# Optimization experiments

Hardware: AMD Instinct MI355X
Metric: run time of the kernel (lower is better)

Reference implementation:

```python
import jax, jax.numpy as jnp
import numpy as np

# MoE config (matches init_kwargs): dim=512, num_experts=16, top_k=2, ffn mult=4
DIM = 512
NUM_EXPERTS = 16
TOP_K = 2
HIDDEN = 4 * DIM  # FeedForward inner dim
TOKENS = 2048
LN_EPS = 1e-5


def setup_inputs() -> dict:
    key = jax.random.key(0)
    ks = jax.random.split(key, 4)
    scaled = lambda k, shape, fan_in: (
        jax.random.normal(k, shape, dtype=jnp.float32) / np.sqrt(fan_in)
    )
    return {
        "x": jax.random.normal(ks[0], (TOKENS, DIM), dtype=jnp.float32),
        # gate: Linear(dim, num_experts, bias=False)
        "Wg": scaled(ks[1], (DIM, NUM_EXPERTS), DIM),
        # per-expert FFN params stacked on leading expert axis
        "W1": scaled(ks[2], (NUM_EXPERTS, DIM, HIDDEN), DIM),
        "b1": jnp.zeros((NUM_EXPERTS, HIDDEN), jnp.float32),
        "ln_g": jnp.ones((NUM_EXPERTS, HIDDEN), jnp.float32),
        "ln_b": jnp.zeros((NUM_EXPERTS, HIDDEN), jnp.float32),
        "W2": scaled(ks[3], (NUM_EXPERTS, HIDDEN, DIM), HIDDEN),
        "b2": jnp.zeros((NUM_EXPERTS, DIM), jnp.float32),
    }


def reference(x, Wg, W1, b1, ln_g, ln_b, W2, b2):
    # ---- routing ----
    gate_logits = x @ Wg                                   # [T, E]
    w, sel = jax.lax.top_k(gate_logits, TOP_K)             # [T, k]
    # softmax over the selected-experts axis, computed in fp32 (matches dtype=torch.float)
    w = jax.nn.softmax(w.astype(jnp.float32), axis=-1).astype(x.dtype)
    n_exp = Wg.shape[1]
    # combine[t, e] = sum_k w[t, k] * 1[sel[t, k] == e]
    combine = jnp.sum(
        w[..., None] * jax.nn.one_hot(sel, n_exp, dtype=x.dtype), axis=1
    )                                                      # [T, E]

    # ---- all experts (dense, jit-friendly dispatch) ----
    # FeedForward: Linear -> SiLU -> LayerNorm -> (Dropout=identity at eval) -> Linear
    h = jnp.einsum("td,edh->eth", x, W1) + b1[:, None, :]  # [E, T, H]
    h = jax.nn.silu(h)
    mu = jnp.mean(h, axis=-1, keepdims=True)
    var = jnp.mean(jnp.square(h - mu), axis=-1, keepdims=True)
    h = (h - mu) * jax.lax.rsqrt(var + LN_EPS)
    h = h * ln_g[:, None, :] + ln_b[:, None, :]
    y = jnp.einsum("eth,ehd->etd", h, W2) + b2[:, None, :]  # [E, T, D]

    # ---- weighted combine (scatter-add equivalent) ----
    return jnp.einsum("etd,te->td", y, combine)             # [T, D]
```

## Files before the change

kernel.cpp:

```cpp
#include <hip/hip_runtime.h>
#include <hip/hip_bf16.h>

#define TOKENS 2048
#define DIM 512
#define NEXP 16
#define HID 2048
#define CAP 320
#define NTPE (CAP / 64)
#define MTILES (NEXP * NTPE)
#define NROWS (NEXP * CAP)

typedef unsigned short ushort_t;
typedef __attribute__((ext_vector_type(8))) __bf16 bf16x8;
typedef __attribute__((ext_vector_type(4))) float f32x4;

#define OFF_CNT 0
#define OFF_LTOK 1024
#define OFF_LW 21504
#define OFF_S1 41984
#define OFF_S2 62464
#define OFF_XBF 82944
#define OFF_H 2180096
#define OFF_W1T 23151616
#define OFF_W2T 56706048

__device__ __forceinline__ ushort_t f2b(float f) {
  __bf16 b = (__bf16)f;
  return __builtin_bit_cast(unsigned short, b);
}
__device__ __forceinline__ float b2f(ushort_t u) {
  return __builtin_bit_cast(float, (unsigned)u << 16);
}


__global__ __launch_bounds__(256) void pre_k(
    const float* __restrict__ x, const float* __restrict__ Wg,
    const float* __restrict__ W1, ushort_t* __restrict__ xbf,
    int* __restrict__ counts, int* __restrict__ ltok, float* __restrict__ lw,
    float* __restrict__ s1, float* __restrict__ s2, float* __restrict__ out,
    ushort_t* __restrict__ W1t) {
  int bid = blockIdx.x;
  int t = threadIdx.x;
  if (bid >= 64) {
    int idx = bid - 64;
    int xcd = idx & 7;
    int j = idx >> 3;
    int e = ((j >> 8) << 3) | xcd;
    int bx = j & 255;
    int bn = bx & 31, bk = bx >> 5;
    const int K = DIM, N = HID;
    int w = t >> 6, l = t & 63;
    int n = bn * 64 + l;
    int k_base = bk * 64, kt0 = k_base >> 5, kk = w * 8;
    const float* sp = W1 + ((size_t)e * K + k_base + kk) * N + n;
    float v[16];
#pragma unroll
    for (int jj = 0; jj < 8; jj++)
      v[jj] = __builtin_nontemporal_load(sp + (size_t)jj * N);
#pragma unroll
    for (int jj = 0; jj < 8; jj++)
      v[8 + jj] = __builtin_nontemporal_load(sp + (size_t)(32 + jj) * N);
    size_t tb = ((size_t)(e * (N >> 4) + (n >> 4)) * (K >> 5) + kt0) * 512 +
                (n & 15) * 32 + kk;
    union { ushort_t u[8]; uint4 q; } s0, s1u;
#pragma unroll
    for (int jj = 0; jj < 8; jj++) { s0.u[jj] = f2b(v[jj]); s1u.u[jj] = f2b(v[8 + jj]); }
    *(uint4*)(W1t + tb) = s0.q;
    *(uint4*)(W1t + tb + 512) = s1u.q;
    return;
  }

  {
    float4 z = {0.f, 0.f, 0.f, 0.f};
    float4* o4 = (float4*)out + bid * 4096 + t;
#pragma unroll
    for (int i = 0; i < 16; i++) o4[i * 256] = z;
  }
  {
    int idx = bid * 256 + t;
    if (idx < NROWS) { s1[idx] = 0.f; s2[idx] = 0.f; }
  }

  __shared__ float xs[4][512];
  __shared__ float lg[4][16];
  __shared__ int lcnt[NEXP];
  __shared__ int ltoks[NEXP][64];
  __shared__ float lws[NEXP][64];
  __shared__ int base_s[NEXP];

  if (t < NEXP) lcnt[t] = 0;
  __syncthreads();

  int lane = t & 63, w = t >> 6;
  int dq = lane >> 2, e4 = lane & 3;
  const float* wgp = Wg + dq * NEXP + e4 * 4;

  for (int it = 0; it < 8; it++) {
    int tok = bid * 32 + w * 8 + it;
    const float* xr = x + (size_t)tok * DIM + lane * 8;
    float4 xa = *(const float4*)xr;
    float4 xb = *(const float4*)(xr + 4);
    union { ushort_t u[8]; uint4 v; } pk;
    pk.u[0] = f2b(xa.x); pk.u[1] = f2b(xa.y); pk.u[2] = f2b(xa.z); pk.u[3] = f2b(xa.w);
    pk.u[4] = f2b(xb.x); pk.u[5] = f2b(xb.y); pk.u[6] = f2b(xb.z); pk.u[7] = f2b(xb.w);
    *(uint4*)(xbf + (size_t)tok * DIM + lane * 8) = pk.v;
    *(float4*)&xs[w][lane * 8] = xa;
    *(float4*)&xs[w][lane * 8 + 4] = xb;

    float4 a = {0.f, 0.f, 0.f, 0.f};
#pragma unroll
    for (int kk = 0; kk < 32; kk++) {
      float xv = xs[w][kk * 16 + dq];
      float4 g = *(const float4*)(wgp + kk * 16 * NEXP);
      a.x += xv * g.x; a.y += xv * g.y; a.z += xv * g.z; a.w += xv * g.w;
    }
#pragma unroll
    for (int off = 32; off >= 4; off >>= 1) {
      a.x += __shfl_down(a.x, off);
      a.y += __shfl_down(a.y, off);
      a.z += __shfl_down(a.z, off);
      a.w += __shfl_down(a.w, off);
    }
    if (lane < 4) *(float4*)&lg[w][lane * 4] = a;
    if (lane == 0) {
      int i0 = 0;
      float v0 = lg[w][0];
#pragma unroll
      for (int e = 1; e < NEXP; e++)
        if (lg[w][e] > v0) { v0 = lg[w][e]; i0 = e; }
      int i1 = -1;
      float v1 = -3.4e38f;
#pragma unroll
      for (int e = 0; e < NEXP; e++)
        if (e != i0 && lg[w][e] > v1) { v1 = lg[w][e]; i1 = e; }
      float ex = __expf(v1 - v0);
      float w0 = 1.f / (1.f + ex);
      int p0 = atomicAdd(&lcnt[i0], 1);
      ltoks[i0][p0] = tok;
      lws[i0][p0] = w0;
      int p1 = atomicAdd(&lcnt[i1], 1);
      ltoks[i1][p1] = tok;
      lws[i1][p1] = ex / (1.f + ex);
    }
  }
  __syncthreads();
  if (t < NEXP) base_s[t] = atomicAdd(&counts[t], lcnt[t]);
  __syncthreads();
  int e = t >> 4, i0 = t & 15;
  int n = lcnt[e], b = base_s[e];
  for (int i = i0; i < n; i += 16) {
    int slot = b + i;
    if (slot < CAP) {
      ltok[e * CAP + slot] = ltoks[e][i];
      lw[e * CAP + slot] = lws[e][i];
    }
  }
}

__global__ __launch_bounds__(256) void mid_k(
    const ushort_t* __restrict__ W1t, const float* __restrict__ b1,
    const int* __restrict__ counts, const int* __restrict__ ltok,
    const ushort_t* __restrict__ xbf, ushort_t* __restrict__ hbuf,
    float* __restrict__ s1, float* __restrict__ s2,
    const float* __restrict__ W2, ushort_t* __restrict__ W2t) {
  int bid = blockIdx.x;
  int t = threadIdx.x;
  if (bid >= 640) {
    int idx = bid - 640;
    int xcd = idx & 7;
    int j = idx >> 3;
    int e = ((j >> 8) << 3) | xcd;
    int bx = j & 255;
    int bn = bx & 7, bk = bx >> 3;
    const int K = HID, N = DIM;
    int w = t >> 6, l = t & 63;
    int n = bn * 64 + l;
    int k_base = bk * 64, kt0 = k_base >> 5, kk = w * 8;
    const float* sp = W2 + ((size_t)e * K + k_base + kk) * N + n;
    float v[16];
#pragma unroll
    for (int jj = 0; jj < 8; jj++)
      v[jj] = __builtin_nontemporal_load(sp + (size_t)jj * N);
#pragma unroll
    for (int jj = 0; jj < 8; jj++)
      v[8 + jj] = __builtin_nontemporal_load(sp + (size_t)(32 + jj) * N);
    size_t tb = ((size_t)(e * (N >> 4) + (n >> 4)) * (K >> 5) + kt0) * 512 +
                (n & 15) * 32 + kk;
    union { ushort_t u[8]; uint4 q; } s0, s1u;
#pragma unroll
    for (int jj = 0; jj < 8; jj++) { s0.u[jj] = f2b(v[jj]); s1u.u[jj] = f2b(v[8 + jj]); }
    *(uint4*)(W2t + tb) = s0.q;
    *(uint4*)(W2t + tb + 512) = s1u.q;
    return;
  }

  int xcd = bid & 7;
  int j = bid >> 3;
  int e = ((j / 40) << 3) | xcd;
  int r = j % 40;
  int mt = r >> 3;
  int h0 = (r & 7) * 256;
  int cnt = counts[e];
  if (cnt - mt * 64 <= 0) return;
  int row0 = e * CAP + mt * 64;

  __shared__ __align__(16) ushort_t As[2][64 * 40];

  int lane = t & 63, wave = t >> 6;
  int quad = lane >> 4, l16 = lane & 15;

  int sr = t >> 2, sp = t & 3;
  int stok = ltok[row0 + sr];
  bool sok = (unsigned)stok < TOKENS;
  const ushort_t* sx = xbf + (size_t)(sok ? stok : 0) * DIM + sp * 8;

  int ncol = h0 + wave * 64 + l16;
  const ushort_t* bb = W1t +
      ((size_t)(e * 128 + (h0 >> 4) + wave * 4) * 16) * 512 + l16 * 32 + quad * 8;

  f32x4 acc[4][4];
#pragma unroll
  for (int a = 0; a < 4; a++)
#pragma unroll
    for (int b = 0; b < 4; b++) acc[a][b] = {0.f, 0.f, 0.f, 0.f};

  uint4 avB = {0u, 0u, 0u, 0u};
  {
    uint4 avA = {0u, 0u, 0u, 0u};
    if (sok) {
      avA = *(const uint4*)(sx);
      avB = *(const uint4*)(sx + 32);
    }
    *(uint4*)(&As[0][sr * 40 + sp * 8]) = avA;
  }
  bf16x8 bc[4];
#pragma unroll
  for (int nb = 0; nb < 4; nb++)
    bc[nb] = *(const bf16x8*)(bb + nb * 8192);

#pragma unroll
  for (int ks = 0; ks < 16; ks++) {
    __syncthreads();
    bf16x8 bn[4];
    if (ks < 15) {
#pragma unroll
      for (int nb = 0; nb < 4; nb++)
        bn[nb] = *(const bf16x8*)(bb + nb * 8192 + (ks + 1) * 512);
    }
    uint4 avN = {0u, 0u, 0u, 0u};
    if (ks < 14 && sok) avN = *(const uint4*)(sx + (ks + 2) * 32);

    bf16x8 af[4];
#pragma unroll
    for (int mb = 0; mb < 4; mb++)
      af[mb] = *(const bf16x8*)(&As[ks & 1][(mb * 16 + l16) * 40 + quad * 8]);
#pragma unroll
    for (int mb = 0; mb < 4; mb++)
#pragma unroll
      for (int nb = 0; nb < 4; nb++)
        acc[mb][nb] = __builtin_amdgcn_mfma_f32_16x16x32_bf16(af[mb], bc[nb], acc[mb][nb], 0, 0, 0);

    if (ks < 15) {
      *(uint4*)(&As[(ks + 1) & 1][sr * 40 + sp * 8]) = avB;
      avB = avN;
#pragma unroll
      for (int nb = 0; nb < 4; nb++) bc[nb] = bn[nb];
    }
  }

  float bia[4];
#pragma unroll
  for (int nb = 0; nb < 4; nb++) bia[nb] = b1[e * HID + ncol + nb * 16];
#pragma unroll
  for (int mb = 0; mb < 4; mb++) {
#pragma unroll
    for (int i = 0; i < 4; i++) {
      int m = mb * 16 + quad * 4 + i;
      size_t rowg = (size_t)(row0 + m);
      float ps = 0.f, qs = 0.f;
#pragma unroll
      for (int nb = 0; nb < 4; nb++) {
        float v = acc[mb][nb][i] + bia[nb];
        v = v / (1.f + __expf(-v));
        hbuf[rowg * HID + ncol + nb * 16] = f2b(v);
        ps += v;
        qs += v * v;
      }
      ps += __shfl_down(ps, 8); qs += __shfl_down(qs, 8);
      ps += __shfl_down(ps, 4); qs += __shfl_down(qs, 4);
      ps += __shfl_down(ps, 2); qs += __shfl_down(qs, 2);
      ps += __shfl_down(ps, 1); qs += __shfl_down(qs, 1);
      if (l16 == 0) {
        atomicAdd(&s1[rowg], ps);
        atomicAdd(&s2[rowg], qs);
      }
    }
  }
}

__global__ __launch_bounds__(256) void ffn2_k(
    const ushort_t* __restrict__ W2t, const float* __restrict__ b2,
    const float* __restrict__ lng, const float* __restrict__ lnb,
    const int* __restrict__ counts, const int* __restrict__ ltok,
    const float* __restrict__ lw, const ushort_t* __restrict__ hbuf,
    const float* __restrict__ s1, const float* __restrict__ s2,
    float* __restrict__ out) {
  int bid = blockIdx.x;
  int xcd = bid & 7, j = bid >> 3;
  int eh = j / 40, r = j % 40;
  int e = (eh << 3) | xcd;
  int mt = r % 5, yz = r / 5;
  int n0 = (yz >> 1) * 128;
  int z = yz & 1;
  int kbeg = z * (HID / 2);

  int cnt = counts[e];
  int valid = cnt - mt * 64;
  if (valid <= 0) return;
  valid = valid > 64 ? 64 : valid;
  int row0 = e * CAP + mt * 64;

  __shared__ __align__(16) ushort_t As[2][64 * 40];
  __shared__ float Gs[1024];
  __shared__ float Cs[1024];

  int t = threadIdx.x;
  int lane = t & 63, wave = t >> 6;
  int quad = lane >> 4, l16 = lane & 15;

  *(float4*)&Gs[t * 4] = *(const float4*)(lng + (size_t)e * HID + kbeg + t * 4);
  *(float4*)&Cs[t * 4] = *(const float4*)(lnb + (size_t)e * HID + kbeg + t * 4);

  int sr = t >> 2, sp = t & 3;
  size_t srow = (size_t)(row0 + sr);
  const ushort_t* hr = hbuf + srow * HID + kbeg + sp * 8;
  float smu = s1[srow] * (1.f / HID);
  float var = s2[srow] * (1.f / HID) - smu * smu;
  float srs = rsqrtf(var + 1e-5f);

  int ncol = n0 + wave * 32 + l16;
  const ushort_t* bb = W2t +
      ((size_t)(e * 32 + (n0 >> 4) + wave * 2) * 64 + z * 32) * 512 +
      l16 * 32 + quad * 8;

  f32x4 acc[4][2];
#pragma unroll
  for (int a = 0; a < 4; a++)
#pragma unroll
    for (int b = 0; b < 2; b++) acc[a][b] = {0.f, 0.f, 0.f, 0.f};

  uint4 hvA = *(const uint4*)(hr);
  uint4 hvB = *(const uint4*)(hr + 32);
  __syncthreads();

  {
    union { uint4 v; ushort_t u[8]; } hv;
    hv.v = hvA;
    int sb = sp * 8;
    union { ushort_t u[8]; uint4 v; } pk;
#pragma unroll
    for (int jj = 0; jj < 8; jj++) {
      float f = (b2f(hv.u[jj]) - smu) * srs;
      pk.u[jj] = f2b(f * Gs[sb + jj] + Cs[sb + jj]);
    }
    *(uint4*)(&As[0][sr * 40 + sp * 8]) = pk.v;
  }
  bf16x8 bc[2];
#pragma unroll
  for (int nb = 0; nb < 2; nb++)
    bc[nb] = *(const bf16x8*)(bb + nb * 32768);

#pragma unroll 8
  for (int ks = 0; ks < 32; ks++) {
    __syncthreads();
    bf16x8 bn[2];
    if (ks < 31) {
#pragma unroll
      for (int nb = 0; nb < 2; nb++)
        bn[nb] = *(const bf16x8*)(bb + nb * 32768 + (ks + 1) * 512);
    }
    uint4 hvN = {0u, 0u, 0u, 0u};
    if (ks < 30) hvN = *(const uint4*)(hr + (ks + 2) * 32);

    bf16x8 af[4];
#pragma unroll
    for (int mb = 0; mb < 4; mb++)
      af[mb] = *(const bf16x8*)(&As[ks & 1][(mb * 16 + l16) * 40 + quad * 8]);
#pragma unroll
    for (int mb = 0; mb < 4; mb++)
#pragma unroll
      for (int nb = 0; nb < 2; nb++)
        acc[mb][nb] = __builtin_amdgcn_mfma_f32_16x16x32_bf16(af[mb], bc[nb], acc[mb][nb], 0, 0, 0);

    if (ks < 31) {
      union { uint4 v; ushort_t u[8]; } hv;
      hv.v = hvB;
      int sb = (ks + 1) * 32 + sp * 8;
      union { ushort_t u[8]; uint4 v; } pk;
#pragma unroll
      for (int jj = 0; jj < 8; jj++) {
        float f = (b2f(hv.u[jj]) - smu) * srs;
        pk.u[jj] = f2b(f * Gs[sb + jj] + Cs[sb + jj]);
      }
      *(uint4*)(&As[(ks + 1) & 1][sr * 40 + sp * 8]) = pk.v;
      hvB = hvN;
#pragma unroll
      for (int nb = 0; nb < 2; nb++) bc[nb] = bn[nb];
    }
  }

  bool addb = (z == 0);
  float bia[2];
#pragma unroll
  for (int nb = 0; nb < 2; nb++)
    bia[nb] = addb ? b2[e * DIM + ncol + nb * 16] : 0.f;
#pragma unroll
  for (int mb = 0; mb < 4; mb++) {
#pragma unroll
    for (int i = 0; i < 4; i++) {
      int m = mb * 16 + quad * 4 + i;
      if (m < valid) {
        int tok = ltok[row0 + m];
        float w = lw[row0 + m];
#pragma unroll
        for (int nb = 0; nb < 2; nb++) {
          float v = acc[mb][nb][i] + bia[nb];
          atomicAdd(out + (size_t)tok * DIM + ncol + nb * 16, w * v);
        }
      }
    }
  }
}

extern "C" void kernel_launch(void* const* d_in, const int* in_sizes, int n_in,
                              void* d_out, int out_size, void* d_ws, size_t ws_size,
                              hipStream_t stream) {
  const float* x = (const float*)d_in[0];
  const float* Wg = (const float*)d_in[1];
  const float* W1 = (const float*)d_in[2];
  const float* b1 = (const float*)d_in[3];
  const float* lng = (const float*)d_in[4];
  const float* lnb = (const float*)d_in[5];
  const float* W2 = (const float*)d_in[6];
  const float* b2 = (const float*)d_in[7];
  float* out = (float*)d_out;

  char* ws = (char*)d_ws;
  int* counts = (int*)(ws + OFF_CNT);
  int* ltok = (int*)(ws + OFF_LTOK);
  float* lw = (float*)(ws + OFF_LW);
  float* s1 = (float*)(ws + OFF_S1);
  float* s2 = (float*)(ws + OFF_S2);
  ushort_t* xbf = (ushort_t*)(ws + OFF_XBF);
  ushort_t* hbuf = (ushort_t*)(ws + OFF_H);
  ushort_t* W1t = (ushort_t*)(ws + OFF_W1T);
  ushort_t* W2t = (ushort_t*)(ws + OFF_W2T);

  hipMemsetAsync(counts, 0, NEXP * sizeof(int), stream);
  pre_k<<<64 + 4096, 256, 0, stream>>>(x, Wg, W1, xbf, counts, ltok, lw,
                                       s1, s2, out, W1t);
  mid_k<<<640 + 4096, 256, 0, stream>>>(W1t, b1, counts, ltok, xbf, hbuf,
                                        s1, s2, W2, W2t);
  ffn2_k<<<640, 256, 0, stream>>>(W2t, b2, lng, lnb, counts, ltok, lw,
                                  hbuf, s1, s2, out);
}
```

Before: 235.0 us.

## Read fp32 expert weights directly in GEMMs, drop separate bf16 repack passes

Removes the blocks that converted W1 and W2 from fp32 to a tiled bf16 layout in workspace. The FFN GEMM kernels now load fp32 weights straight from the input with strided per-column loads and convert to bf16 in registers before the MFMA. This cuts a full write plus re-read of both weight tensors (about 128MB fp32 read, 64MB bf16 written then read). The cost is uncoalesced-ish strided scalar loads, more VGPRs for the fp32 prefetch buffers, and each weight element being read by several M-tiles in fp32 rather than bf16.

```diff
diff --git a/kernel.cpp b/kernel.cpp
--- a/kernel.cpp
+++ b/kernel.cpp
@@ -7,7 +7,6 @@
 #define HID 2048
 #define CAP 320
 #define NTPE (CAP / 64)
-#define MTILES (NEXP * NTPE)
 #define NROWS (NEXP * CAP)
 
 typedef unsigned short ushort_t;
@@ -21,8 +20,6 @@
 #define OFF_S2 62464
 #define OFF_XBF 82944
 #define OFF_H 2180096
-#define OFF_W1T 23151616
-#define OFF_W2T 56706048
 
 __device__ __forceinline__ ushort_t f2b(float f) {
   __bf16 b = (__bf16)f;
@@ -33,51 +30,20 @@
 }
 
 
-__global__ __launch_bounds__(256) void pre_k(
+__global__ __launch_bounds__(256) void router_k(
     const float* __restrict__ x, const float* __restrict__ Wg,
-    const float* __restrict__ W1, ushort_t* __restrict__ xbf,
-    int* __restrict__ counts, int* __restrict__ ltok, float* __restrict__ lw,
-    float* __restrict__ s1, float* __restrict__ s2, float* __restrict__ out,
-    ushort_t* __restrict__ W1t) {
-  int bid = blockIdx.x;
+    ushort_t* __restrict__ xbf, int* __restrict__ counts,
+    int* __restrict__ ltok, float* __restrict__ lw,
+    float* __restrict__ s1, float* __restrict__ s2, float* __restrict__ out) {
   int t = threadIdx.x;
-  if (bid >= 64) {
-    int idx = bid - 64;
-    int xcd = idx & 7;
-    int j = idx >> 3;
-    int e = ((j >> 8) << 3) | xcd;
-    int bx = j & 255;
-    int bn = bx & 31, bk = bx >> 5;
-    const int K = DIM, N = HID;
-    int w = t >> 6, l = t & 63;
-    int n = bn * 64 + l;
-    int k_base = bk * 64, kt0 = k_base >> 5, kk = w * 8;
-    const float* sp = W1 + ((size_t)e * K + k_base + kk) * N + n;
-    float v[16];
-#pragma unroll
-    for (int jj = 0; jj < 8; jj++)
-      v[jj] = __builtin_nontemporal_load(sp + (size_t)jj * N);
-#pragma unroll
-    for (int jj = 0; jj < 8; jj++)
-      v[8 + jj] = __builtin_nontemporal_load(sp + (size_t)(32 + jj) * N);
-    size_t tb = ((size_t)(e * (N >> 4) + (n >> 4)) * (K >> 5) + kt0) * 512 +
-                (n & 15) * 32 + kk;
-    union { ushort_t u[8]; uint4 q; } s0, s1u;
-#pragma unroll
-    for (int jj = 0; jj < 8; jj++) { s0.u[jj] = f2b(v[jj]); s1u.u[jj] = f2b(v[8 + jj]); }
-    *(uint4*)(W1t + tb) = s0.q;
-    *(uint4*)(W1t + tb + 512) = s1u.q;
-    return;
-  }
-
   {
     float4 z = {0.f, 0.f, 0.f, 0.f};
-    float4* o4 = (float4*)out + bid * 4096 + t;
+    float4* o4 = (float4*)out + blockIdx.x * 4096 + t;
 #pragma unroll
     for (int i = 0; i < 16; i++) o4[i * 256] = z;
   }
   {
-    int idx = bid * 256 + t;
+    int idx = blockIdx.x * 256 + t;
     if (idx < NROWS) { s1[idx] = 0.f; s2[idx] = 0.f; }
   }
 
@@ -96,7 +62,7 @@
   const float* wgp = Wg + dq * NEXP + e4 * 4;
 
   for (int it = 0; it < 8; it++) {
-    int tok = bid * 32 + w * 8 + it;
+    int tok = blockIdx.x * 32 + w * 8 + it;
     const float* xr = x + (size_t)tok * DIM + lane * 8;
     float4 xa = *(const float4*)xr;
     float4 xb = *(const float4*)(xr + 4);
@@ -157,43 +123,13 @@
   }
 }
 
-__global__ __launch_bounds__(256) void mid_k(
-    const ushort_t* __restrict__ W1t, const float* __restrict__ b1,
+__global__ __launch_bounds__(256) void ffn1_k(
+    const float* __restrict__ W1, const float* __restrict__ b1,
     const int* __restrict__ counts, const int* __restrict__ ltok,
     const ushort_t* __restrict__ xbf, ushort_t* __restrict__ hbuf,
-    float* __restrict__ s1, float* __restrict__ s2,
-    const float* __restrict__ W2, ushort_t* __restrict__ W2t) {
+    float* __restrict__ s1, float* __restrict__ s2) {
   int bid = blockIdx.x;
   int t = threadIdx.x;
-  if (bid >= 640) {
-    int idx = bid - 640;
-    int xcd = idx & 7;
-    int j = idx >> 3;
-    int e = ((j >> 8) << 3) | xcd;
-    int bx = j & 255;
-    int bn = bx & 7, bk = bx >> 3;
-    const int K = HID, N = DIM;
-    int w = t >> 6, l = t & 63;
-    int n = bn * 64 + l;
-    int k_base = bk * 64, kt0 = k_base >> 5, kk = w * 8;
-    const float* sp = W2 + ((size_t)e * K + k_base + kk) * N + n;
-    float v[16];
-#pragma unroll
-    for (int jj = 0; jj < 8; jj++)
-      v[jj] = __builtin_nontemporal_load(sp + (size_t)jj * N);
-#pragma unroll
-    for (int jj = 0; jj < 8; jj++)
-      v[8 + jj] = __builtin_nontemporal_load(sp + (size_t)(32 + jj) * N);
-    size_t tb = ((size_t)(e * (N >> 4) + (n >> 4)) * (K >> 5) + kt0) * 512 +
-                (n & 15) * 32 + kk;
-    union { ushort_t u[8]; uint4 q; } s0, s1u;
-#pragma unroll
-    for (int jj = 0; jj < 8; jj++) { s0.u[jj] = f2b(v[jj]); s1u.u[jj] = f2b(v[8 + jj]); }
-    *(uint4*)(W2t + tb) = s0.q;
-    *(uint4*)(W2t + tb + 512) = s1u.q;
-    return;
-  }
-
   int xcd = bid & 7;
   int j = bid >> 3;
   int e = ((j / 40) << 3) | xcd;
@@ -215,8 +151,7 @@
   const ushort_t* sx = xbf + (size_t)(sok ? stok : 0) * DIM + sp * 8;
 
   int ncol = h0 + wave * 64 + l16;
-  const ushort_t* bb = W1t +
-      ((size_t)(e * 128 + (h0 >> 4) + wave * 4) * 16) * 512 + l16 * 32 + quad * 8;
+  const float* wb = W1 + ((size_t)e * DIM + quad * 8) * HID + ncol;
 
   f32x4 acc[4][4];
 #pragma unroll
@@ -233,22 +168,35 @@
     }
     *(uint4*)(&As[0][sr * 40 + sp * 8]) = avA;
   }
-  bf16x8 bc[4];
+  float bcf[4][8];
 #pragma unroll
   for (int nb = 0; nb < 4; nb++)
-    bc[nb] = *(const bf16x8*)(bb + nb * 8192);
+#pragma unroll
+    for (int jj = 0; jj < 8; jj++)
+      bcf[nb][jj] = wb[(size_t)jj * HID + nb * 16];
 
 #pragma unroll
   for (int ks = 0; ks < 16; ks++) {
     __syncthreads();
-    bf16x8 bn[4];
+    float bnf[4][8];
     if (ks < 15) {
 #pragma unroll
       for (int nb = 0; nb < 4; nb++)
-        bn[nb] = *(const bf16x8*)(bb + nb * 8192 + (ks + 1) * 512);
+#pragma unroll
+        for (int jj = 0; jj < 8; jj++)
+          bnf[nb][jj] = wb[(size_t)((ks + 1) * 32 + jj) * HID + nb * 16];
     }
     uint4 avN = {0u, 0u, 0u, 0u};
     if (ks < 14 && sok) avN = *(const uint4*)(sx + (ks + 2) * 32);
+
+    bf16x8 bc[4];
+#pragma unroll
+    for (int nb = 0; nb < 4; nb++) {
+      union { ushort_t u[8]; bf16x8 f; } o;
+#pragma unroll
+      for (int jj = 0; jj < 8; jj++) o.u[jj] = f2b(bcf[nb][jj]);
+      bc[nb] = o.f;
+    }
 
     bf16x8 af[4];
 #pragma unroll
@@ -264,7 +212,9 @@
       *(uint4*)(&As[(ks + 1) & 1][sr * 40 + sp * 8]) = avB;
       avB = avN;
 #pragma unroll
-      for (int nb = 0; nb < 4; nb++) bc[nb] = bn[nb];
+      for (int nb = 0; nb < 4; nb++)
+#pragma unroll
+        for (int jj = 0; jj < 8; jj++) bcf[nb][jj] = bnf[nb][jj];
     }
   }
 
@@ -299,7 +249,7 @@
 }
 
 __global__ __launch_bounds__(256) void ffn2_k(
-    const ushort_t* __restrict__ W2t, const float* __restrict__ b2,
+    const float* __restrict__ W2, const float* __restrict__ b2,
     const float* __restrict__ lng, const float* __restrict__ lnb,
     const int* __restrict__ counts, const int* __restrict__ ltok,
     const float* __restrict__ lw, const ushort_t* __restrict__ hbuf,
@@ -339,9 +289,7 @@
   float srs = rsqrtf(var + 1e-5f);
 
   int ncol = n0 + wave * 32 + l16;
-  const ushort_t* bb = W2t +
-      ((size_t)(e * 32 + (n0 >> 4) + wave * 2) * 64 + z * 32) * 512 +
-      l16 * 32 + quad * 8;
+  const float* wb2 = W2 + ((size_t)e * HID + kbeg + quad * 8) * DIM + ncol;
 
   f32x4 acc[4][2];
 #pragma unroll
@@ -365,22 +313,35 @@
     }
     *(uint4*)(&As[0][sr * 40 + sp * 8]) = pk.v;
   }
-  bf16x8 bc[2];
+  float bcf[2][8];
 #pragma unroll
   for (int nb = 0; nb < 2; nb++)
-    bc[nb] = *(const bf16x8*)(bb + nb * 32768);
+#pragma unroll
+    for (int jj = 0; jj < 8; jj++)
+      bcf[nb][jj] = wb2[(size_t)jj * DIM + nb * 16];
 
 #pragma unroll 8
   for (int ks = 0; ks < 32; ks++) {
     __syncthreads();
-    bf16x8 bn[2];
+    float bnf[2][8];
     if (ks < 31) {
 #pragma unroll
       for (int nb = 0; nb < 2; nb++)
-        bn[nb] = *(const bf16x8*)(bb + nb * 32768 + (ks + 1) * 512);
+#pragma unroll
+        for (int jj = 0; jj < 8; jj++)
+          bnf[nb][jj] = wb2[(size_t)((ks + 1) * 32 + jj) * DIM + nb * 16];
     }
     uint4 hvN = {0u, 0u, 0u, 0u};
     if (ks < 30) hvN = *(const uint4*)(hr + (ks + 2) * 32);
+
+    bf16x8 bc[2];
+#pragma unroll
+    for (int nb = 0; nb < 2; nb++) {
+      union { ushort_t u[8]; bf16x8 f; } o;
+#pragma unroll
+      for (int jj = 0; jj < 8; jj++) o.u[jj] = f2b(bcf[nb][jj]);
+      bc[nb] = o.f;
+    }
 
     bf16x8 af[4];
 #pragma unroll
@@ -405,7 +366,9 @@
       *(uint4*)(&As[(ks + 1) & 1][sr * 40 + sp * 8]) = pk.v;
       hvB = hvN;
 #pragma unroll
-      for (int nb = 0; nb < 2; nb++) bc[nb] = bn[nb];
+      for (int nb = 0; nb < 2; nb++)
+#pragma unroll
+        for (int jj = 0; jj < 8; jj++) bcf[nb][jj] = bnf[nb][jj];
     }
   }
 
@@ -453,14 +416,10 @@
   float* s2 = (float*)(ws + OFF_S2);
   ushort_t* xbf = (ushort_t*)(ws + OFF_XBF);
   ushort_t* hbuf = (ushort_t*)(ws + OFF_H);
-  ushort_t* W1t = (ushort_t*)(ws + OFF_W1T);
-  ushort_t* W2t = (ushort_t*)(ws + OFF_W2T);
 
   hipMemsetAsync(counts, 0, NEXP * sizeof(int), stream);
-  pre_k<<<64 + 4096, 256, 0, stream>>>(x, Wg, W1, xbf, counts, ltok, lw,
-                                       s1, s2, out, W1t);
-  mid_k<<<640 + 4096, 256, 0, stream>>>(W1t, b1, counts, ltok, xbf, hbuf,
-                                        s1, s2, W2, W2t);
-  ffn2_k<<<640, 256, 0, stream>>>(W2t, b2, lng, lnb, counts, ltok, lw,
+  router_k<<<64, 256, 0, stream>>>(x, Wg, xbf, counts, ltok, lw, s1, s2, out);
+  ffn1_k<<<640, 256, 0, stream>>>(W1, b1, counts, ltok, xbf, hbuf, s1, s2);
+  ffn2_k<<<640, 256, 0, stream>>>(W2, b2, lng, lnb, counts, ltok, lw,
                                   hbuf, s1, s2, out);
 }
```

After: 249.5 us. +6.2%, slower.
